# Kernel optimization log

Measured on AMD Instinct MI355X. Metric: run time of the kernel, lower is better.

## Reference

```python
import jax, jax.numpy as jnp
import numpy as np

DIM = 1024
NUM_HEADS = 16
HEAD_DIM = DIM // NUM_HEADS  # 64
MAX_LABELS = 8
B, SQ, SKV = 2, 2048, 2048


def setup_inputs() -> dict:
    key = jax.random.key(0)
    ks = jax.random.split(key, 12)
    s = 0.02
    return {
        "visual_features": jax.random.normal(ks[0], (B, SQ, DIM), jnp.float32),
        "audio_features": jax.random.normal(ks[1], (B, SKV, DIM), jnp.float32),
        "audio_labels": jax.random.randint(ks[2], (B,), 0, MAX_LABELS),
        "Wq": jax.random.normal(ks[3], (DIM, DIM), jnp.float32) * s,
        "bq": jnp.zeros((DIM,), jnp.float32),
        "Wk": jax.random.normal(ks[4], (DIM, DIM), jnp.float32) * s,
        "bk": jnp.zeros((DIM,), jnp.float32),
        "Wv": jax.random.normal(ks[5], (DIM, DIM), jnp.float32) * s,
        "bv": jnp.zeros((DIM,), jnp.float32),
        "Wo": jax.random.normal(ks[6], (DIM, DIM), jnp.float32) * s,
        "bo": jnp.zeros((DIM,), jnp.float32),
        "label_emb": jax.random.normal(ks[7], (MAX_LABELS, HEAD_DIM), jnp.float32),
    }


def _lrope_emb(label_emb, labels, seq_len, dtype):
    # inv_freq over head_dim (buffer, recomputed)
    inv_freq = 1.0 / (10000.0 ** (jnp.arange(0, HEAD_DIM, 2, dtype=jnp.float32) / HEAD_DIM))
    pos = jnp.arange(seq_len, dtype=dtype)
    freqs = jnp.outer(pos, inv_freq)                       # [S, hd/2]
    emb = jnp.concatenate([jnp.sin(freqs), jnp.cos(freqs)], axis=-1)  # [S, hd]
    lab = label_emb[labels]                                # [B, hd]
    return emb[None, :, :] * lab[:, None, :]               # [B, S, hd]


def reference(visual_features, audio_features, audio_labels,
              Wq, bq, Wk, bk, Wv, bv, Wo, bo, label_emb):
    b, sq, _ = visual_features.shape
    skv = audio_features.shape[1]
    scale = HEAD_DIM ** -0.5

    q = visual_features @ Wq.T + bq                        # [B, Sq, D]
    k = audio_features @ Wk.T + bk                         # [B, Skv, D]
    v = audio_features @ Wv.T + bv

    q = q.reshape(b, sq, NUM_HEADS, HEAD_DIM)
    k = k.reshape(b, skv, NUM_HEADS, HEAD_DIM)
    v = v.reshape(b, skv, NUM_HEADS, HEAD_DIM)

    # L-RoPE additive embedding on K (per-head broadcast of the head_dim-sized emb)
    emb = _lrope_emb(label_emb, audio_labels, skv, k.dtype)  # [B, Skv, hd]
    k = k + emb[:, :, None, :]

    scores = jnp.einsum('bqhd,bkhd->bhqk', q, k) * scale   # [B, H, Sq, Skv]
    attn = jax.nn.softmax(scores, axis=-1)                 # dropout = identity (eval)
    out = jnp.einsum('bhqk,bkhd->bqhd', attn, v)           # [B, Sq, H, hd]
    out = out.reshape(b, sq, DIM)
    return out @ Wo.T + bo
```

## Files before the change

### kernel.cpp

```cpp
#include <hip/hip_runtime.h>
#include <hip/hip_bf16.h>


typedef short s16x8 __attribute__((ext_vector_type(8)));
typedef float f32x4 __attribute__((ext_vector_type(4)));

__device__ __forceinline__ short f2bf(float f) {
    unsigned u = __float_as_uint(f);
    u = u + 0x7fffu + ((u >> 16) & 1u);
    return (short)(u >> 16);
}

__device__ __forceinline__ unsigned cvtpk(float lo, float hi) {
    unsigned r;
    asm volatile("v_cvt_pk_bf16_f32 %0, %1, %2" : "=v"(r) : "v"(lo), "v"(hi));
    return r;
}

#define GLDS16(g, l)                                                          \
    __builtin_amdgcn_global_load_lds(                                         \
        (const __attribute__((address_space(1))) void*)(g),                   \
        (__attribute__((address_space(3))) void*)(l), 16, 0, 0)

__global__ __launch_bounds__(256)
void cvt_all(const float* __restrict__ vis, const float* __restrict__ aud,
             const float* __restrict__ Wq, const float* __restrict__ Wk,
             const float* __restrict__ Wv, const float* __restrict__ Wo,
             short* __restrict__ visB, short* __restrict__ audB,
             short* __restrict__ WqB, short* __restrict__ WkB,
             short* __restrict__ WvB, short* __restrict__ WoB)
{
    const int bid = blockIdx.x;
    const float* src; short* dst; int vec0;
    if (bid < 2048)      { src = vis; dst = visB; vec0 = bid * 256; }
    else if (bid < 4096) { src = aud; dst = audB; vec0 = (bid - 2048) * 256; }
    else {
        const int r = bid - 4096, w = r >> 9, lb = r & 511;
        vec0 = lb * 256;
        if      (w == 0) { src = Wq; dst = WqB; }
        else if (w == 1) { src = Wk; dst = WkB; }
        else if (w == 2) { src = Wv; dst = WvB; }
        else             { src = Wo; dst = WoB; }
    }
    const int i = (vec0 + threadIdx.x) * 8;
    float4 a = *(const float4*)(src + i);
    float4 b = *(const float4*)(src + i + 4);
    s16x8 o;
    o[0]=f2bf(a.x); o[1]=f2bf(a.y); o[2]=f2bf(a.z); o[3]=f2bf(a.w);
    o[4]=f2bf(b.x); o[5]=f2bf(b.y); o[6]=f2bf(b.z); o[7]=f2bf(b.w);
    *(s16x8*)(dst + i) = o;
}

__global__ __launch_bounds__(256)
void gemm_qkv(const short* __restrict__ visB, const short* __restrict__ audB,
              const short* __restrict__ WqB, const short* __restrict__ WkB,
              const short* __restrict__ WvB,
              const float* __restrict__ bq, const float* __restrict__ bk,
              const float* __restrict__ bv,
              short* __restrict__ outQ, short* __restrict__ outK,
              short* __restrict__ outVt,
              const int* __restrict__ labels, const float* __restrict__ lemb)
{
    __shared__ __align__(16) short As[2][64 * 64];
    __shared__ __align__(16) short Bs[2][128 * 64];
    const int tid  = threadIdx.x;
    const int lane = tid & 63;
    const int wid  = tid >> 6;
    const int q15  = lane & 15;
    const int hi   = lane >> 4;
    const int z    = blockIdx.z;
    const int rowBase = blockIdx.y * 64;
    const int colBase = blockIdx.x * 128;
    const int wr = (wid >> 1) * 32;
    const int wc = (wid & 1) * 64;
    const short* X = (z == 0) ? visB : audB;
    const short* W = (z == 0) ? WqB : (z == 1) ? WkB : WvB;
    const float* bias = (z == 0) ? bq : (z == 1) ? bk : bv;

    f32x4 acc[2][4] = {};

    auto stage = [&](int buf, int k0) {
        #pragma unroll
        for (int c = 0; c < 2; ++c) {
            const int u   = c * 256 + tid;
            const int row = u >> 3;
            const int k8a = (u & 7) ^ (row & 7);
            GLDS16(X + (size_t)(rowBase + row) * 1024 + k0 + k8a * 8,
                   &As[buf][(c * 256 + wid * 64) * 8]);
        }
        #pragma unroll
        for (int c = 0; c < 4; ++c) {
            const int u   = c * 256 + tid;
            const int row = u >> 3;
            const int k8a = (u & 7) ^ (row & 7);
            GLDS16(W + (size_t)(colBase + row) * 1024 + k0 + k8a * 8,
                   &Bs[buf][(c * 256 + wid * 64) * 8]);
        }
    };

    stage(0, 0);
    __syncthreads();

    for (int t = 0; t < 16; ++t) {
        const int cur = t & 1;
        if (t < 15) stage(cur ^ 1, (t + 1) * 64);
        #pragma unroll
        for (int ks = 0; ks < 2; ++ks) {
            const int kb = ks * 64 + (hi << 4);
            s16x8 af[2], bfv[4];
            #pragma unroll
            for (int m = 0; m < 2; ++m) {
                const int row = wr + m * 16 + q15;
                af[m] = *(const s16x8*)((const char*)&As[cur][0] + row * 128 + (kb ^ ((row & 7) << 4)));
            }
            #pragma unroll
            for (int n = 0; n < 4; ++n) {
                const int row = wc + n * 16 + q15;
                bfv[n] = *(const s16x8*)((const char*)&Bs[cur][0] + row * 128 + (kb ^ ((row & 7) << 4)));
            }
            #pragma unroll
            for (int m = 0; m < 2; ++m)
                #pragma unroll
                for (int n = 0; n < 4; ++n)
                    acc[m][n] = __builtin_amdgcn_mfma_f32_16x16x32_bf16(af[m], bfv[n], acc[m][n], 0, 0, 0);
        }
        __syncthreads();
    }

    if (z == 2) {
        __syncthreads();
        char* tb = (char*)&As[0][0] + wid * 4096;
        const int b  = rowBase >> 11;
        const int h  = (colBase + wc) >> 6;
        const int kvbase = (rowBase & 2047) + wr;
        #pragma unroll
        for (int m = 0; m < 2; ++m) {
            #pragma unroll
            for (int r = 0; r < 4; ++r) {
                const int kvl = m * 16 + hi * 4 + r;
                #pragma unroll
                for (int n = 0; n < 4; ++n) {
                    const int hd = n * 16 + q15;
                    const float v = acc[m][n][r] + bias[colBase + wc + hd];
                    *(short*)(tb + hd * 64 + ((kvl * 2) ^ ((hd & 3) << 4))) = f2bf(v);
                }
            }
        }
        asm volatile("s_waitcnt lgkmcnt(0)" ::: "memory");
        #pragma unroll
        for (int c = 0; c < 4; ++c) {
            const int u  = c * 64 + lane;
            const int hd = u >> 2;
            const int kc = u & 3;
            s16x8 vv = *(const s16x8*)(tb + hd * 64 + ((kc * 16) ^ ((hd & 3) << 4)));
            *(s16x8*)(outVt + ((size_t)(b * 16 + h) * 64 + hd) * 2048 + kvbase + kc * 8) = vv;
        }
    } else {
        short* Co = (z == 0) ? outQ : outK;
        #pragma unroll
        for (int m = 0; m < 2; ++m) {
            #pragma unroll
            for (int r = 0; r < 4; ++r) {
                const int grow = rowBase + wr + m * 16 + hi * 4 + r;
                #pragma unroll
                for (int n = 0; n < 4; ++n) {
                    const int gcol = colBase + wc + n * 16 + q15;
                    float v = acc[m][n][r] + bias[gcol];
                    if (z == 0) {
                        v *= 0.125f;
                    } else {
                        const int bb = grow >> 11;
                        const int ss = grow & 2047;
                        const int hd = gcol & 63;
                        const int fi = hd & 31;
                        const float ang = (float)ss * __expf((float)fi * (-9.210340371976184f / 32.0f));
                        const float tr  = (hd < 32) ? sinf(ang) : cosf(ang);
                        v += tr * lemb[labels[bb] * 64 + hd];
                    }
                    Co[(size_t)grow * 1024 + gcol] = f2bf(v);
                }
            }
        }
    }
}

__global__ __launch_bounds__(256)
void gemm_out(const short* __restrict__ X, const short* __restrict__ W,
              const float* __restrict__ bias, float* __restrict__ Cf)
{
    __shared__ __align__(16) short As[2][64 * 64];
    __shared__ __align__(16) short Bs[2][128 * 64];
    const int tid  = threadIdx.x;
    const int lane = tid & 63;
    const int wid  = tid >> 6;
    const int q15  = lane & 15;
    const int hi   = lane >> 4;
    const int rowBase = blockIdx.y * 64;
    const int colBase = blockIdx.x * 128;
    const int wr = (wid >> 1) * 32;
    const int wc = (wid & 1) * 64;

    f32x4 acc[2][4] = {};

    auto stage = [&](int buf, int k0) {
        #pragma unroll
        for (int c = 0; c < 2; ++c) {
            const int u   = c * 256 + tid;
            const int row = u >> 3;
            const int k8a = (u & 7) ^ (row & 7);
            GLDS16(X + (size_t)(rowBase + row) * 1024 + k0 + k8a * 8,
                   &As[buf][(c * 256 + wid * 64) * 8]);
        }
        #pragma unroll
        for (int c = 0; c < 4; ++c) {
            const int u   = c * 256 + tid;
            const int row = u >> 3;
            const int k8a = (u & 7) ^ (row & 7);
            GLDS16(W + (size_t)(colBase + row) * 1024 + k0 + k8a * 8,
                   &Bs[buf][(c * 256 + wid * 64) * 8]);
        }
    };

    stage(0, 0);
    __syncthreads();

    for (int t = 0; t < 16; ++t) {
        const int cur = t & 1;
        if (t < 15) stage(cur ^ 1, (t + 1) * 64);
        #pragma unroll
        for (int ks = 0; ks < 2; ++ks) {
            const int kb = ks * 64 + (hi << 4);
            s16x8 af[2], bfv[4];
            #pragma unroll
            for (int m = 0; m < 2; ++m) {
                const int row = wr + m * 16 + q15;
                af[m] = *(const s16x8*)((const char*)&As[cur][0] + row * 128 + (kb ^ ((row & 7) << 4)));
            }
            #pragma unroll
            for (int n = 0; n < 4; ++n) {
                const int row = wc + n * 16 + q15;
                bfv[n] = *(const s16x8*)((const char*)&Bs[cur][0] + row * 128 + (kb ^ ((row & 7) << 4)));
            }
            #pragma unroll
            for (int m = 0; m < 2; ++m)
                #pragma unroll
                for (int n = 0; n < 4; ++n)
                    acc[m][n] = __builtin_amdgcn_mfma_f32_16x16x32_bf16(af[m], bfv[n], acc[m][n], 0, 0, 0);
        }
        __syncthreads();
    }

    #pragma unroll
    for (int m = 0; m < 2; ++m) {
        #pragma unroll
        for (int r = 0; r < 4; ++r) {
            const int grow = rowBase + wr + m * 16 + hi * 4 + r;
            #pragma unroll
            for (int n = 0; n < 4; ++n) {
                const int gcol = colBase + wc + n * 16 + q15;
                Cf[(size_t)grow * 1024 + gcol] = acc[m][n][r] + bias[gcol];
            }
        }
    }
}

__global__ __launch_bounds__(256)
void attn_fwd(const short* __restrict__ Q, const short* __restrict__ K,
              const short* __restrict__ Vt, short* __restrict__ AO)
{
    __shared__ __align__(16) short Ks[2][64 * 64];
    __shared__ __align__(16) short Vs[2][64 * 64];
    __shared__ __align__(16) short Ps[4][16 * 64];
    const int tid  = threadIdx.x;
    const int lane = tid & 63;
    const int wid  = tid >> 6;
    const int q15  = lane & 15;
    const int hi   = lane >> 4;
    const int qt = blockIdx.x;
    const int bh = blockIdx.y;
    const int b  = bh >> 4, h = bh & 15;
    const int qrow0 = b * 2048 + qt * 64;
    const int hoff  = h * 64;
    const short* Kb = K + (size_t)b * 2048 * 1024 + hoff;
    const short* Vb = Vt + (size_t)bh * 64 * 2048;
    char* pw = (char*)&Ps[wid][0];
    const int psw = (q15 & 7) << 4;

    s16x8 qf[2];
    {
        const int qr = qrow0 + wid * 16 + q15;
        const short* qp = Q + (size_t)qr * 1024 + hoff + hi * 8;
        qf[0] = *(const s16x8*)(qp);
        qf[1] = *(const s16x8*)(qp + 32);
    }

    auto stage = [&](int buf, int kv0) {
        #pragma unroll
        for (int c = 0; c < 2; ++c) {
            const int ub  = c * 256 + wid * 64;
            const int u   = ub + lane;
            const int row = u >> 3;
            const int k8  = (u & 7) ^ (row & 7);
            GLDS16(Kb + (size_t)(kv0 + row) * 1024 + k8 * 8, &Ks[buf][ub * 8]);
            GLDS16(Vb + (size_t)row * 2048 + kv0 + k8 * 8,   &Vs[buf][ub * 8]);
        }
    };

    float mrun = -1e30f, lsum = 0.f;
    f32x4 o[4] = {};

    stage(0, 0);
    __syncthreads();

    for (int t = 0; t < 32; ++t) {
        const int cur = t & 1;
        if (t < 31) stage(cur ^ 1, (t + 1) * 64);

        f32x4 s[4] = {};
        #pragma unroll
        for (int ks = 0; ks < 2; ++ks) {
            const int kb = ks * 64 + (hi << 4);
            #pragma unroll
            for (int n = 0; n < 4; ++n) {
                const int row = n * 16 + q15;
                s16x8 kf = *(const s16x8*)((const char*)&Ks[cur][0] + row * 128 + (kb ^ ((row & 7) << 4)));
                s[n] = __builtin_amdgcn_mfma_f32_16x16x32_bf16(kf, qf[ks], s[n], 0, 0, 0);
            }
        }

        float pm = s[0][0];
        #pragma unroll
        for (int n = 0; n < 4; ++n)
            #pragma unroll
            for (int r = 0; r < 4; ++r) pm = fmaxf(pm, s[n][r]);
        if (__any(pm > mrun + 8.0f)) {
            float t2 = fmaxf(pm, __shfl_xor(pm, 16));
            t2 = fmaxf(t2, __shfl_xor(t2, 32));
            const float mn = fmaxf(mrun, t2);
            const float al = __expf(mrun - mn);
            mrun = mn;
            lsum *= al;
            float alq[4];
            #pragma unroll
            for (int r = 0; r < 4; ++r) alq[r] = __shfl(al, hi * 4 + r);
            #pragma unroll
            for (int n = 0; n < 4; ++n)
                #pragma unroll
                for (int r = 0; r < 4; ++r) o[n][r] *= alq[r];
        }
        #pragma unroll
        for (int n = 0; n < 4; ++n) {
            float p0 = __expf(s[n][0] - mrun);
            float p1 = __expf(s[n][1] - mrun);
            float p2 = __expf(s[n][2] - mrun);
            float p3 = __expf(s[n][3] - mrun);
            lsum += (p0 + p1) + (p2 + p3);
            uint2 pk;
            pk.x = cvtpk(p0, p1);
            pk.y = cvtpk(p2, p3);
            *(uint2*)(pw + q15 * 128 + ((n * 32 + hi * 8) ^ psw)) = pk;
        }
        asm volatile("s_waitcnt lgkmcnt(0)" ::: "memory");

        #pragma unroll
        for (int ks = 0; ks < 2; ++ks) {
            const int kb = ks * 64 + (hi << 4);
            s16x8 pa = *(const s16x8*)(pw + q15 * 128 + ((ks * 64 + hi * 16) ^ psw));
            #pragma unroll
            for (int n = 0; n < 4; ++n) {
                const int row = n * 16 + q15;
                s16x8 vb = *(const s16x8*)((const char*)&Vs[cur][0] + row * 128 + (kb ^ ((row & 7) << 4)));
                o[n] = __builtin_amdgcn_mfma_f32_16x16x32_bf16(pa, vb, o[n], 0, 0, 0);
            }
        }
        __syncthreads();
    }

    float tt = lsum;
    tt += __shfl_xor(tt, 16);
    tt += __shfl_xor(tt, 32);
    const float inv = 1.0f / tt;
    float invq[4];
    #pragma unroll
    for (int r = 0; r < 4; ++r) invq[r] = __shfl(inv, hi * 4 + r);
    #pragma unroll
    for (int r = 0; r < 4; ++r) {
        const int grow = qrow0 + wid * 16 + hi * 4 + r;
        #pragma unroll
        for (int n = 0; n < 4; ++n) {
            const int gcol = hoff + n * 16 + q15;
            AO[(size_t)grow * 1024 + gcol] = f2bf(o[n][r] * invq[r]);
        }
    }
}

extern "C" void kernel_launch(void* const* d_in, const int* in_sizes, int n_in,
                              void* d_out, int out_size, void* d_ws, size_t ws_size,
                              hipStream_t stream) {
    const float* vis    = (const float*)d_in[0];
    const float* aud    = (const float*)d_in[1];
    const int*   labels = (const int*)d_in[2];
    const float* Wq = (const float*)d_in[3];  const float* bq = (const float*)d_in[4];
    const float* Wk = (const float*)d_in[5];  const float* bk = (const float*)d_in[6];
    const float* Wv = (const float*)d_in[7];  const float* bv = (const float*)d_in[8];
    const float* Wo = (const float*)d_in[9];  const float* bo = (const float*)d_in[10];
    const float* lemb = (const float*)d_in[11];

    short* wsQ   = (short*)d_ws;
    short* wsK   = wsQ  + 4194304;
    short* wsVt  = wsK  + 4194304;
    short* wsAO  = wsVt + 4194304;
    short* visB  = wsAO + 4194304;
    short* audB  = visB + 4194304;
    short* WqB   = audB + 4194304;
    short* WkB   = WqB  + 1048576;
    short* WvB   = WkB  + 1048576;
    short* WoB   = WvB  + 1048576;
    float* out   = (float*)d_out;

    cvt_all<<<6144, 256, 0, stream>>>(vis, aud, Wq, Wk, Wv, Wo,
                                      visB, audB, WqB, WkB, WvB, WoB);
    gemm_qkv<<<dim3(8, 64, 3), 256, 0, stream>>>(visB, audB, WqB, WkB, WvB,
                                                 bq, bk, bv, wsQ, wsK, wsVt,
                                                 labels, lemb);
    attn_fwd<<<dim3(32, 32), 256, 0, stream>>>(wsQ, wsK, wsVt, wsAO);
    gemm_out<<<dim3(8, 64), 256, 0, stream>>>(wsAO, WoB, bo, out);
}
```

Baseline: 248.9 us.

## Switch attention to 32x32 MFMA with register P, enlarge QKV tiles, swizzle blocks

Attention now gives each wave 32 query rows and uses 32x32x16 bf16 MFMAs. The P matrix is repacked in registers with permlane32 swaps instead of a round trip through LDS, and each block covers 128 queries. The QKV GEMM moves to 128x128 tiles with single-buffered LDS. Both GEMMs and attention gain a block-index remap aimed at L2 locality. The GEMMs lose the double-buffer overlap of loads with compute, in exchange for more reuse per tile and a single-buffered LDS footprint.

```diff
diff --git a/kernel.cpp b/kernel.cpp
--- a/kernel.cpp
+++ b/kernel.cpp
@@ -4,6 +4,8 @@
 
 typedef short s16x8 __attribute__((ext_vector_type(8)));
 typedef float f32x4 __attribute__((ext_vector_type(4)));
+typedef float f32x16 __attribute__((ext_vector_type(16)));
+typedef unsigned uintx4 __attribute__((ext_vector_type(4)));
 
 __device__ __forceinline__ short f2bf(float f) {
     unsigned u = __float_as_uint(f);
@@ -16,6 +18,8 @@
     asm volatile("v_cvt_pk_bf16_f32 %0, %1, %2" : "=v"(r) : "v"(lo), "v"(hi));
     return r;
 }
+
+#define PLSWAP(a, b) asm volatile("v_permlane32_swap_b32 %0, %1" : "+v"(a), "+v"(b))
 
 #define GLDS16(g, l)                                                          \
     __builtin_amdgcn_global_load_lds(                                         \
@@ -61,80 +65,71 @@
               short* __restrict__ outVt,
               const int* __restrict__ labels, const float* __restrict__ lemb)
 {
-    __shared__ __align__(16) short As[2][64 * 64];
-    __shared__ __align__(16) short Bs[2][128 * 64];
+    __shared__ __align__(16) short SM[16384];
+    short* As = SM;
+    short* Bs = SM + 8192;
     const int tid  = threadIdx.x;
     const int lane = tid & 63;
     const int wid  = tid >> 6;
     const int q15  = lane & 15;
     const int hi   = lane >> 4;
-    const int z    = blockIdx.z;
-    const int rowBase = blockIdx.y * 64;
-    const int colBase = blockIdx.x * 128;
-    const int wr = (wid >> 1) * 32;
+    const int lid = blockIdx.x + 8 * blockIdx.y + 256 * blockIdx.z;
+    const int wk  = (lid & 7) * 96 + (lid >> 3);
+    const int z   = wk >> 8;
+    const int rowBase = ((wk >> 3) & 31) * 128;
+    const int colBase = (wk & 7) * 128;
+    const int wr = (wid >> 1) * 64;
     const int wc = (wid & 1) * 64;
     const short* X = (z == 0) ? visB : audB;
     const short* W = (z == 0) ? WqB : (z == 1) ? WkB : WvB;
     const float* bias = (z == 0) ? bq : (z == 1) ? bk : bv;
 
-    f32x4 acc[2][4] = {};
-
-    auto stage = [&](int buf, int k0) {
-        #pragma unroll
-        for (int c = 0; c < 2; ++c) {
-            const int u   = c * 256 + tid;
+    f32x4 acc[4][4] = {};
+
+    for (int t = 0; t < 16; ++t) {
+        const int k0 = t * 64;
+        __syncthreads();
+        #pragma unroll
+        for (int c = 0; c < 4; ++c) {
+            const int u   = (wid * 4 + c) * 64 + lane;
             const int row = u >> 3;
             const int k8a = (u & 7) ^ (row & 7);
             GLDS16(X + (size_t)(rowBase + row) * 1024 + k0 + k8a * 8,
-                   &As[buf][(c * 256 + wid * 64) * 8]);
-        }
-        #pragma unroll
-        for (int c = 0; c < 4; ++c) {
-            const int u   = c * 256 + tid;
-            const int row = u >> 3;
-            const int k8a = (u & 7) ^ (row & 7);
+                   As + (wid * 4 + c) * 512);
             GLDS16(W + (size_t)(colBase + row) * 1024 + k0 + k8a * 8,
-                   &Bs[buf][(c * 256 + wid * 64) * 8]);
-        }
-    };
-
-    stage(0, 0);
-    __syncthreads();
-
-    for (int t = 0; t < 16; ++t) {
-        const int cur = t & 1;
-        if (t < 15) stage(cur ^ 1, (t + 1) * 64);
+                   Bs + (wid * 4 + c) * 512);
+        }
+        __syncthreads();
         #pragma unroll
         for (int ks = 0; ks < 2; ++ks) {
             const int kb = ks * 64 + (hi << 4);
-            s16x8 af[2], bfv[4];
-            #pragma unroll
-            for (int m = 0; m < 2; ++m) {
+            s16x8 af[4], bfv[4];
+            #pragma unroll
+            for (int m = 0; m < 4; ++m) {
                 const int row = wr + m * 16 + q15;
-                af[m] = *(const s16x8*)((const char*)&As[cur][0] + row * 128 + (kb ^ ((row & 7) << 4)));
+                af[m] = *(const s16x8*)((const char*)As + row * 128 + (kb ^ ((row & 7) << 4)));
             }
             #pragma unroll
             for (int n = 0; n < 4; ++n) {
                 const int row = wc + n * 16 + q15;
-                bfv[n] = *(const s16x8*)((const char*)&Bs[cur][0] + row * 128 + (kb ^ ((row & 7) << 4)));
-            }
-            #pragma unroll
-            for (int m = 0; m < 2; ++m)
+                bfv[n] = *(const s16x8*)((const char*)Bs + row * 128 + (kb ^ ((row & 7) << 4)));
+            }
+            #pragma unroll
+            for (int m = 0; m < 4; ++m)
                 #pragma unroll
                 for (int n = 0; n < 4; ++n)
                     acc[m][n] = __builtin_amdgcn_mfma_f32_16x16x32_bf16(af[m], bfv[n], acc[m][n], 0, 0, 0);
         }
-        __syncthreads();
     }
 
     if (z == 2) {
         __syncthreads();
-        char* tb = (char*)&As[0][0] + wid * 4096;
+        char* tb = (char*)SM + wid * 8192;
         const int b  = rowBase >> 11;
         const int h  = (colBase + wc) >> 6;
         const int kvbase = (rowBase & 2047) + wr;
         #pragma unroll
-        for (int m = 0; m < 2; ++m) {
+        for (int m = 0; m < 4; ++m) {
             #pragma unroll
             for (int r = 0; r < 4; ++r) {
                 const int kvl = m * 16 + hi * 4 + r;
@@ -142,23 +137,23 @@
                 for (int n = 0; n < 4; ++n) {
                     const int hd = n * 16 + q15;
                     const float v = acc[m][n][r] + bias[colBase + wc + hd];
-                    *(short*)(tb + hd * 64 + ((kvl * 2) ^ ((hd & 3) << 4))) = f2bf(v);
+                    *(short*)(tb + hd * 128 + ((kvl * 2) ^ ((hd & 7) << 4))) = f2bf(v);
                 }
             }
         }
         asm volatile("s_waitcnt lgkmcnt(0)" ::: "memory");
         #pragma unroll
-        for (int c = 0; c < 4; ++c) {
+        for (int c = 0; c < 8; ++c) {
             const int u  = c * 64 + lane;
-            const int hd = u >> 2;
-            const int kc = u & 3;
-            s16x8 vv = *(const s16x8*)(tb + hd * 64 + ((kc * 16) ^ ((hd & 3) << 4)));
+            const int hd = u >> 3;
+            const int kc = u & 7;
+            s16x8 vv = *(const s16x8*)(tb + hd * 128 + ((kc * 16) ^ ((hd & 7) << 4)));
             *(s16x8*)(outVt + ((size_t)(b * 16 + h) * 64 + hd) * 2048 + kvbase + kc * 8) = vv;
         }
     } else {
         short* Co = (z == 0) ? outQ : outK;
         #pragma unroll
-        for (int m = 0; m < 2; ++m) {
+        for (int m = 0; m < 4; ++m) {
             #pragma unroll
             for (int r = 0; r < 4; ++r) {
                 const int grow = rowBase + wr + m * 16 + hi * 4 + r;
@@ -188,28 +183,33 @@
 void gemm_out(const short* __restrict__ X, const short* __restrict__ W,
               const float* __restrict__ bias, float* __restrict__ Cf)
 {
-    __shared__ __align__(16) short As[2][64 * 64];
-    __shared__ __align__(16) short Bs[2][128 * 64];
+    __shared__ __align__(16) short SM[12288];
+    short* As = SM;
+    short* Bs = SM + 4096;
     const int tid  = threadIdx.x;
     const int lane = tid & 63;
     const int wid  = tid >> 6;
     const int q15  = lane & 15;
     const int hi   = lane >> 4;
-    const int rowBase = blockIdx.y * 64;
-    const int colBase = blockIdx.x * 128;
+    const int lid = blockIdx.x + 8 * blockIdx.y;
+    const int wk  = (lid & 7) * 64 + (lid >> 3);
+    const int rowBase = (wk >> 3) * 64;
+    const int colBase = (wk & 7) * 128;
     const int wr = (wid >> 1) * 32;
     const int wc = (wid & 1) * 64;
 
     f32x4 acc[2][4] = {};
 
-    auto stage = [&](int buf, int k0) {
+    for (int t = 0; t < 16; ++t) {
+        const int k0 = t * 64;
+        __syncthreads();
         #pragma unroll
         for (int c = 0; c < 2; ++c) {
             const int u   = c * 256 + tid;
             const int row = u >> 3;
             const int k8a = (u & 7) ^ (row & 7);
             GLDS16(X + (size_t)(rowBase + row) * 1024 + k0 + k8a * 8,
-                   &As[buf][(c * 256 + wid * 64) * 8]);
+                   As + (c * 256 + wid * 64) * 8);
         }
         #pragma unroll
         for (int c = 0; c < 4; ++c) {
@@ -217,16 +217,9 @@
             const int row = u >> 3;
             const int k8a = (u & 7) ^ (row & 7);
             GLDS16(W + (size_t)(colBase + row) * 1024 + k0 + k8a * 8,
-                   &Bs[buf][(c * 256 + wid * 64) * 8]);
-        }
-    };
-
-    stage(0, 0);
-    __syncthreads();
-
-    for (int t = 0; t < 16; ++t) {
-        const int cur = t & 1;
-        if (t < 15) stage(cur ^ 1, (t + 1) * 64);
+                   Bs + (c * 256 + wid * 64) * 8);
+        }
+        __syncthreads();
         #pragma unroll
         for (int ks = 0; ks < 2; ++ks) {
             const int kb = ks * 64 + (hi << 4);
@@ -234,12 +227,12 @@
             #pragma unroll
             for (int m = 0; m < 2; ++m) {
                 const int row = wr + m * 16 + q15;
-                af[m] = *(const s16x8*)((const char*)&As[cur][0] + row * 128 + (kb ^ ((row & 7) << 4)));
+                af[m] = *(const s16x8*)((const char*)As + row * 128 + (kb ^ ((row & 7) << 4)));
             }
             #pragma unroll
             for (int n = 0; n < 4; ++n) {
                 const int row = wc + n * 16 + q15;
-                bfv[n] = *(const s16x8*)((const char*)&Bs[cur][0] + row * 128 + (kb ^ ((row & 7) << 4)));
+                bfv[n] = *(const s16x8*)((const char*)Bs + row * 128 + (kb ^ ((row & 7) << 4)));
             }
             #pragma unroll
             for (int m = 0; m < 2; ++m)
@@ -247,7 +240,6 @@
                 for (int n = 0; n < 4; ++n)
                     acc[m][n] = __builtin_amdgcn_mfma_f32_16x16x32_bf16(af[m], bfv[n], acc[m][n], 0, 0, 0);
         }
-        __syncthreads();
     }
 
     #pragma unroll
@@ -270,28 +262,26 @@
 {
     __shared__ __align__(16) short Ks[2][64 * 64];
     __shared__ __align__(16) short Vs[2][64 * 64];
-    __shared__ __align__(16) short Ps[4][16 * 64];
     const int tid  = threadIdx.x;
     const int lane = tid & 63;
     const int wid  = tid >> 6;
-    const int q15  = lane & 15;
-    const int hi   = lane >> 4;
-    const int qt = blockIdx.x;
-    const int bh = blockIdx.y;
-    const int b  = bh >> 4, h = bh & 15;
-    const int qrow0 = b * 2048 + qt * 64;
-    const int hoff  = h * 64;
+    const int l31  = lane & 31;
+    const int h    = lane >> 5;
+    const int lid = blockIdx.x + 16 * blockIdx.y;
+    const int wk  = (lid & 7) * 64 + (lid >> 3);
+    const int qt  = wk & 15;
+    const int bh  = wk >> 4;
+    const int b   = bh >> 4, hh = bh & 15;
+    const int qrow0 = b * 2048 + qt * 128 + wid * 32;
+    const int hoff  = hh * 64;
     const short* Kb = K + (size_t)b * 2048 * 1024 + hoff;
     const short* Vb = Vt + (size_t)bh * 64 * 2048;
-    char* pw = (char*)&Ps[wid][0];
-    const int psw = (q15 & 7) << 4;
-
-    s16x8 qf[2];
+
+    s16x8 qf[4];
     {
-        const int qr = qrow0 + wid * 16 + q15;
-        const short* qp = Q + (size_t)qr * 1024 + hoff + hi * 8;
-        qf[0] = *(const s16x8*)(qp);
-        qf[1] = *(const s16x8*)(qp + 32);
+        const short* qp = Q + (size_t)(qrow0 + l31) * 1024 + hoff + h * 8;
+        #pragma unroll
+        for (int st = 0; st < 4; ++st) qf[st] = *(const s16x8*)(qp + st * 16);
     }
 
     auto stage = [&](int buf, int kv0) {
@@ -307,7 +297,7 @@
     };
 
     float mrun = -1e30f, lsum = 0.f;
-    f32x4 o[4] = {};
+    f32x16 o0 = {}, o1 = {};
 
     stage(0, 0);
     __syncthreads();
@@ -316,81 +306,80 @@
         const int cur = t & 1;
         if (t < 31) stage(cur ^ 1, (t + 1) * 64);
 
-        f32x4 s[4] = {};
-        #pragma unroll
-        for (int ks = 0; ks < 2; ++ks) {
-            const int kb = ks * 64 + (hi << 4);
-            #pragma unroll
-            for (int n = 0; n < 4; ++n) {
-                const int row = n * 16 + q15;
-                s16x8 kf = *(const s16x8*)((const char*)&Ks[cur][0] + row * 128 + (kb ^ ((row & 7) << 4)));
-                s[n] = __builtin_amdgcn_mfma_f32_16x16x32_bf16(kf, qf[ks], s[n], 0, 0, 0);
-            }
-        }
-
-        float pm = s[0][0];
-        #pragma unroll
-        for (int n = 0; n < 4; ++n)
-            #pragma unroll
-            for (int r = 0; r < 4; ++r) pm = fmaxf(pm, s[n][r]);
+        f32x16 sA = {}, sB = {};
+        #pragma unroll
+        for (int st = 0; st < 4; ++st) {
+            const int kb = st * 32 + h * 16;
+            const int sw = (l31 & 7) << 4;
+            s16x8 a0 = *(const s16x8*)((const char*)&Ks[cur][0] + l31 * 128 + (kb ^ sw));
+            s16x8 a1 = *(const s16x8*)((const char*)&Ks[cur][0] + (32 + l31) * 128 + (kb ^ sw));
+            sA = __builtin_amdgcn_mfma_f32_32x32x16_bf16(a0, qf[st], sA, 0, 0, 0);
+            sB = __builtin_amdgcn_mfma_f32_32x32x16_bf16(a1, qf[st], sB, 0, 0, 0);
+        }
+
+        float pm = sA[0];
+        #pragma unroll
+        for (int r = 1; r < 16; ++r) pm = fmaxf(pm, sA[r]);
+        #pragma unroll
+        for (int r = 0; r < 16; ++r) pm = fmaxf(pm, sB[r]);
         if (__any(pm > mrun + 8.0f)) {
-            float t2 = fmaxf(pm, __shfl_xor(pm, 16));
-            t2 = fmaxf(t2, __shfl_xor(t2, 32));
-            const float mn = fmaxf(mrun, t2);
+            pm = fmaxf(pm, __shfl_xor(pm, 32));
+            const float mn = fmaxf(mrun, pm);
             const float al = __expf(mrun - mn);
             mrun = mn;
             lsum *= al;
-            float alq[4];
-            #pragma unroll
-            for (int r = 0; r < 4; ++r) alq[r] = __shfl(al, hi * 4 + r);
-            #pragma unroll
-            for (int n = 0; n < 4; ++n)
-                #pragma unroll
-                for (int r = 0; r < 4; ++r) o[n][r] *= alq[r];
-        }
-        #pragma unroll
-        for (int n = 0; n < 4; ++n) {
-            float p0 = __expf(s[n][0] - mrun);
-            float p1 = __expf(s[n][1] - mrun);
-            float p2 = __expf(s[n][2] - mrun);
-            float p3 = __expf(s[n][3] - mrun);
-            lsum += (p0 + p1) + (p2 + p3);
-            uint2 pk;
-            pk.x = cvtpk(p0, p1);
-            pk.y = cvtpk(p2, p3);
-            *(uint2*)(pw + q15 * 128 + ((n * 32 + hi * 8) ^ psw)) = pk;
-        }
-        asm volatile("s_waitcnt lgkmcnt(0)" ::: "memory");
-
-        #pragma unroll
-        for (int ks = 0; ks < 2; ++ks) {
-            const int kb = ks * 64 + (hi << 4);
-            s16x8 pa = *(const s16x8*)(pw + q15 * 128 + ((ks * 64 + hi * 16) ^ psw));
-            #pragma unroll
-            for (int n = 0; n < 4; ++n) {
-                const int row = n * 16 + q15;
-                s16x8 vb = *(const s16x8*)((const char*)&Vs[cur][0] + row * 128 + (kb ^ ((row & 7) << 4)));
-                o[n] = __builtin_amdgcn_mfma_f32_16x16x32_bf16(pa, vb, o[n], 0, 0, 0);
-            }
-        }
-        __syncthreads();
-    }
-
-    float tt = lsum;
-    tt += __shfl_xor(tt, 16);
-    tt += __shfl_xor(tt, 32);
-    const float inv = 1.0f / tt;
-    float invq[4];
+            #pragma unroll
+            for (int reg = 0; reg < 16; ++reg) {
+                const int qsrc = ((reg & 3) + 8 * (reg >> 2)) + 4 * h;
+                const float aq = __shfl(al, qsrc);
+                o0[reg] *= aq;
+                o1[reg] *= aq;
+            }
+        }
+
+        #pragma unroll
+        for (int ks = 0; ks < 4; ++ks) {
+            float p0, p1, p2, p3, p4, p5, p6, p7;
+            if (ks == 0) {
+                p0=__expf(sA[0]-mrun); p1=__expf(sA[1]-mrun); p2=__expf(sA[2]-mrun); p3=__expf(sA[3]-mrun);
+                p4=__expf(sA[4]-mrun); p5=__expf(sA[5]-mrun); p6=__expf(sA[6]-mrun); p7=__expf(sA[7]-mrun);
+            } else if (ks == 1) {
+                p0=__expf(sA[8]-mrun); p1=__expf(sA[9]-mrun); p2=__expf(sA[10]-mrun); p3=__expf(sA[11]-mrun);
+                p4=__expf(sA[12]-mrun); p5=__expf(sA[13]-mrun); p6=__expf(sA[14]-mrun); p7=__expf(sA[15]-mrun);
+            } else if (ks == 2) {
+                p0=__expf(sB[0]-mrun); p1=__expf(sB[1]-mrun); p2=__expf(sB[2]-mrun); p3=__expf(sB[3]-mrun);
+                p4=__expf(sB[4]-mrun); p5=__expf(sB[5]-mrun); p6=__expf(sB[6]-mrun); p7=__expf(sB[7]-mrun);
+            } else {
+                p0=__expf(sB[8]-mrun); p1=__expf(sB[9]-mrun); p2=__expf(sB[10]-mrun); p3=__expf(sB[11]-mrun);
+                p4=__expf(sB[12]-mrun); p5=__expf(sB[13]-mrun); p6=__expf(sB[14]-mrun); p7=__expf(sB[15]-mrun);
+            }
+            lsum += ((p0 + p1) + (p2 + p3)) + ((p4 + p5) + (p6 + p7));
+            unsigned E0 = cvtpk(p0, p1), E1 = cvtpk(p2, p3);
+            unsigned O0 = cvtpk(p4, p5), O1 = cvtpk(p6, p7);
+            PLSWAP(E0, O0);
+            PLSWAP(E1, O1);
+            uintx4 fr = {E0, E1, O0, O1};
+            s16x8 pa = __builtin_bit_cast(s16x8, fr);
+
+            const int kb = ks * 32 + h * 16;
+            const int sw = (l31 & 7) << 4;
+            s16x8 vb0 = *(const s16x8*)((const char*)&Vs[cur][0] + l31 * 128 + (kb ^ sw));
+            s16x8 vb1 = *(const s16x8*)((const char*)&Vs[cur][0] + (32 + l31) * 128 + (kb ^ sw));
+            o0 = __builtin_amdgcn_mfma_f32_32x32x16_bf16(pa, vb0, o0, 0, 0, 0);
+            o1 = __builtin_amdgcn_mfma_f32_32x32x16_bf16(pa, vb1, o1, 0, 0, 0);
+        }
+        __syncthreads();
+    }
+
+    const float ltot = lsum + __shfl_xor(lsum, 32);
+    const float inv = 1.0f / ltot;
     #pragma unroll
-    for (int r = 0; r < 4; ++r) invq[r] = __shfl(inv, hi * 4 + r);
-    #pragma unroll
-    for (int r = 0; r < 4; ++r) {
-        const int grow = qrow0 + wid * 16 + hi * 4 + r;
-        #pragma unroll
-        for (int n = 0; n < 4; ++n) {
-            const int gcol = hoff + n * 16 + q15;
-            AO[(size_t)grow * 1024 + gcol] = f2bf(o[n][r] * invq[r]);
-        }
+    for (int reg = 0; reg < 16; ++reg) {
+        const int crow = (reg & 3) + 8 * (reg >> 2) + 4 * h;
+        const float iq = __shfl(inv, crow);
+        const int grow = qrow0 + crow;
+        AO[(size_t)grow * 1024 + hoff + l31]      = f2bf(o0[reg] * iq);
+        AO[(size_t)grow * 1024 + hoff + 32 + l31] = f2bf(o1[reg] * iq);
     }
 }
 
@@ -420,9 +409,9 @@
 
     cvt_all<<<6144, 256, 0, stream>>>(vis, aud, Wq, Wk, Wv, Wo,
                                       visB, audB, WqB, WkB, WvB, WoB);
-    gemm_qkv<<<dim3(8, 64, 3), 256, 0, stream>>>(visB, audB, WqB, WkB, WvB,
+    gemm_qkv<<<dim3(8, 32, 3), 256, 0, stream>>>(visB, audB, WqB, WkB, WvB,
                                                  bq, bk, bv, wsQ, wsK, wsVt,
                                                  labels, lemb);
-    attn_fwd<<<dim3(32, 32), 256, 0, stream>>>(wsQ, wsK, wsVt, wsAO);
+    attn_fwd<<<dim3(16, 32), 256, 0, stream>>>(wsQ, wsK, wsVt, wsAO);
     gemm_out<<<dim3(8, 64), 256, 0, stream>>>(wsAO, WoB, bo, out);
 }
```

Result: slower. 256.9 us (+3.2%).
